# Performance work log

Measured on AMD Instinct MI355X. Metric: run time of the kernel, lower is better.

The kernel has to match this reference:

```python
import jax, jax.numpy as jnp
import numpy as np
import math

E = 1024   # embed_dim
H = 16     # num_heads
LAT = 1024 # latent_dim
P = LAT // 16  # projectionMatrice output dim (per-head width)
B = 2
S = 2048


def setup_inputs() -> dict:
    key = jax.random.key(0)
    ks = jax.random.split(key, 11)
    sc = 0.02  # small init scale so exp(dot(q_vec, k_vec)) stays finite
    return {
        "x": jax.random.normal(ks[0], (B, S, E), jnp.float32),
        "WQ": jax.random.normal(ks[1], (E, E), jnp.float32) * sc,
        "WK": jax.random.normal(ks[2], (E, E), jnp.float32) * sc,
        "WV": jax.random.normal(ks[3], (E, E), jnp.float32) * sc,
        "result_weight": jax.random.normal(ks[4], (E, E), jnp.float32) * sc,
        "proj_w": jax.random.normal(ks[5], (E, P), jnp.float32) * sc,
        "proj_b": jax.random.normal(ks[6], (P,), jnp.float32) * sc,
        "q1_vector": jax.random.normal(ks[7], (E,), jnp.float32) * sc,
        "k1_vector": jax.random.normal(ks[8], (E,), jnp.float32) * sc,
        "q2_vector": jax.random.normal(ks[9], (E,), jnp.float32) * sc,
        "k2_vector": jax.random.normal(ks[10], (E,), jnp.float32) * sc,
        "lambda_init": jnp.zeros((1,), jnp.float32),
    }


def reference(x, WQ, WK, WV, result_weight, proj_w, proj_b,
              q1_vector, k1_vector, q2_vector, k2_vector, lambda_init):
    head_dim = E // H
    scale = 1.0 / math.sqrt(head_dim)
    # projectionMatrice(x @ W): torch Linear -> x @ proj_w + proj_b with proj_w [E, P]
    q = (x @ WQ) @ proj_w + proj_b   # [B, S, P]
    k = (x @ WK) @ proj_w + proj_b   # [B, S, P]
    v = (x @ WV) @ proj_w + proj_b   # [B, S, P]
    q1, q2 = jnp.split(q, 2, axis=-1)  # [B, S, P/2] each
    k1, k2 = jnp.split(k, 2, axis=-1)
    lam = (jnp.exp(jnp.dot(q1_vector, k1_vector))
           - jnp.exp(jnp.dot(q2_vector, k2_vector)) + lambda_init[0])
    attn1 = jnp.einsum('bsp,btp->bst', q1, k1) * scale  # [B, S, S]
    attn2 = jnp.einsum('bsp,btp->bst', q2, k2) * scale
    base = jnp.einsum('bst,btp->bsp', attn1 - lam * attn2, v)  # [B, S, P]
    # Stateful KV-cache grows by one identical (key, value) copy per head call;
    # head i's tiled-cache output equals (i+1) * base (exact reassociation).
    mult = jnp.arange(1, H + 1, dtype=x.dtype)  # [H]
    heads = (base[:, :, None, :] * mult[None, None, :, None]).reshape(B, S, H * P)  # [B, S, E]
    return heads @ result_weight
```

## Files before the change

### kernel.cpp

```cpp
#include <hip/hip_runtime.h>
#include <hip/hip_bf16.h>


typedef __attribute__((ext_vector_type(8))) short short8;
typedef __attribute__((ext_vector_type(4))) float f32x4;
typedef unsigned short ushort_t;
typedef unsigned int uint_t;

__device__ inline ushort_t f2bf(float v) {
    uint_t u = __float_as_uint(v);
    return (ushort_t)((u + 0x7FFF + ((u >> 16) & 1)) >> 16);
}
__device__ inline float bf2f(ushort_t h) { return __uint_as_float(((uint_t)h) << 16); }
__device__ inline void split2(float v, ushort_t& hi, ushort_t& lo) {
    hi = f2bf(v);
    lo = f2bf(v - bf2f(hi));
}
__device__ inline int swzA(int row, int k) { return (row * 64 + k) ^ ((row & 7) << 3); }

__global__ __launch_bounds__(256) void prep_sk(
    const float* __restrict__ WQ, const float* __restrict__ WK, const float* __restrict__ WV,
    const float* __restrict__ proj_w, float* __restrict__ wppartT)
{
    __shared__ __align__(16) ushort_t Ah[4096], Al[4096], Bh[4096], Bl[4096];
    int bid = blockIdx.x;
    int slice = bid / 48, t = bid % 48, z = t / 16, rowblk = t % 16;
    const float* A = ((z == 0) ? WQ : (z == 1) ? WK : WV) + (long long)rowblk * 64 * 1024;

    int tid = threadIdx.x;
    int wave = tid >> 6, lane = tid & 63;
    int rl = lane & 15, kg = lane >> 4;
    f32x4 acc[4] = {};

    int k0 = slice * 128;
    for (int ch = 0; ch < 2; ++ch, k0 += 64) {
        #pragma unroll
        for (int i = 0; i < 4; ++i) {
            int pos = tid + 256 * i;
            int r = pos >> 4, k4 = (pos & 15) * 4;
            float4 v = *(const float4*)&A[(long long)r * 1024 + k0 + k4];
            ushort4 h, l;
            split2(v.x, h.x, l.x); split2(v.y, h.y, l.y);
            split2(v.z, h.z, l.z); split2(v.w, h.w, l.w);
            int idx = swzA(r, k4);
            *(ushort4*)&Ah[idx] = h;
            *(ushort4*)&Al[idx] = l;
        }
        #pragma unroll
        for (int i = 0; i < 4; ++i) {
            int pos = tid + 256 * i;
            int kk = pos >> 4, n4 = (pos & 15) * 4;
            float4 v = *(const float4*)&proj_w[(long long)(k0 + kk) * 64 + n4];
            float vv[4] = {v.x, v.y, v.z, v.w};
            #pragma unroll
            for (int j = 0; j < 4; ++j) {
                ushort_t h, l; split2(vv[j], h, l);
                int idx = swzA(n4 + j, kk);
                Bh[idx] = h; Bl[idx] = l;
            }
        }
        __syncthreads();
        int ar = wave * 16 + rl;
        #pragma unroll
        for (int ks = 0; ks < 2; ++ks) {
            int kb = ks * 32 + kg * 8;
            short8 ah = *(const short8*)&Ah[swzA(ar, kb)];
            short8 al = *(const short8*)&Al[swzA(ar, kb)];
            #pragma unroll
            for (int n = 0; n < 4; ++n) {
                int bi = swzA(n * 16 + rl, kb);
                short8 bh = *(const short8*)&Bh[bi];
                short8 bl = *(const short8*)&Bl[bi];
                acc[n] = __builtin_amdgcn_mfma_f32_16x16x32_bf16(ah, bh, acc[n], 0, 0, 0);
                acc[n] = __builtin_amdgcn_mfma_f32_16x16x32_bf16(ah, bl, acc[n], 0, 0, 0);
                acc[n] = __builtin_amdgcn_mfma_f32_16x16x32_bf16(al, bh, acc[n], 0, 0, 0);
            }
        }
        __syncthreads();
    }
    #pragma unroll
    for (int n = 0; n < 4; ++n) {
        int col = n * 16 + rl;
        float4 o = {acc[n][0], acc[n][1], acc[n][2], acc[n][3]};
        long long idx = (long long)slice * 196608 + (long long)(z * 64 + col) * 1024
                      + rowblk * 64 + wave * 16 + kg * 4;
        *(float4*)&wppartT[idx] = o;
    }
}

__global__ __launch_bounds__(256) void wpfix2(
    const float* __restrict__ wppartT,
    ushort_t* __restrict__ WpThi, ushort_t* __restrict__ WpTlo)
{
    int idx = blockIdx.x * 256 + threadIdx.x;
    long long off = (long long)idx * 4;
    float4 s = {0.f, 0.f, 0.f, 0.f};
    #pragma unroll
    for (int sl = 0; sl < 8; ++sl) {
        float4 m = *(const float4*)&wppartT[(long long)sl * 196608 + off];
        s.x += m.x; s.y += m.y; s.z += m.z; s.w += m.w;
    }
    ushort4 h, l;
    split2(s.x, h.x, l.x); split2(s.y, h.y, l.y);
    split2(s.z, h.z, l.z); split2(s.w, h.w, l.w);
    *(ushort4*)&WpThi[off] = h;
    *(ushort4*)&WpTlo[off] = l;
}

__global__ __launch_bounds__(256) void qkv2(
    const float* __restrict__ x,
    const ushort_t* __restrict__ WpThi, const ushort_t* __restrict__ WpTlo,
    const float* __restrict__ proj_b,
    ushort_t* __restrict__ Qhi, ushort_t* __restrict__ Qlo,
    float* __restrict__ kbuf, float* __restrict__ vbuf)
{
    __shared__ __align__(16) ushort_t Ah[4096], Al[4096], Bh[4096], Bl[4096];
    int bid = blockIdx.x, tid = threadIdx.x;
    int z = bid >> 6, rowblk = bid & 63;
    long long row0 = (long long)rowblk * 64;
    int wave = tid >> 6, lane = tid & 63, rl = lane & 15, kg = lane >> 4;
    f32x4 acc[4] = {};
    float4 av[4];
    short8 pbh[2], pbl[2];
    #pragma unroll
    for (int i = 0; i < 4; ++i) {
        int pos = tid + 256 * i;
        int r = pos >> 4, c4 = (pos & 15) * 4;
        av[i] = *(const float4*)&x[(row0 + r) * 1024 + c4];
    }
    #pragma unroll
    for (int i = 0; i < 2; ++i) {
        int pos = tid + 256 * i;
        int n = pos >> 3, k8 = (pos & 7) * 8;
        long long src = (long long)(z * 64 + n) * 1024 + k8;
        pbh[i] = *(const short8*)&WpThi[src];
        pbl[i] = *(const short8*)&WpTlo[src];
    }
    for (int ch = 0; ch < 16; ++ch) {
        #pragma unroll
        for (int i = 0; i < 4; ++i) {
            int pos = tid + 256 * i;
            int r = pos >> 4, c4 = (pos & 15) * 4;
            ushort4 h, l;
            split2(av[i].x, h.x, l.x); split2(av[i].y, h.y, l.y);
            split2(av[i].z, h.z, l.z); split2(av[i].w, h.w, l.w);
            int idx = swzA(r, c4);
            *(ushort4*)&Ah[idx] = h;
            *(ushort4*)&Al[idx] = l;
        }
        #pragma unroll
        for (int i = 0; i < 2; ++i) {
            int pos = tid + 256 * i;
            int n = pos >> 3, k8 = (pos & 7) * 8;
            int idx = swzA(n, k8);
            *(short8*)&Bh[idx] = pbh[i];
            *(short8*)&Bl[idx] = pbl[i];
        }
        __syncthreads();
        if (ch < 15) {
            int k0 = (ch + 1) * 64;
            #pragma unroll
            for (int i = 0; i < 4; ++i) {
                int pos = tid + 256 * i;
                int r = pos >> 4, c4 = (pos & 15) * 4;
                av[i] = *(const float4*)&x[(row0 + r) * 1024 + k0 + c4];
            }
            #pragma unroll
            for (int i = 0; i < 2; ++i) {
                int pos = tid + 256 * i;
                int n = pos >> 3, k8 = (pos & 7) * 8;
                long long src = (long long)(z * 64 + n) * 1024 + k0 + k8;
                pbh[i] = *(const short8*)&WpThi[src];
                pbl[i] = *(const short8*)&WpTlo[src];
            }
        }
        int ar = wave * 16 + rl;
        #pragma unroll
        for (int ks = 0; ks < 2; ++ks) {
            int kb = ks * 32 + kg * 8;
            short8 ah = *(const short8*)&Ah[swzA(ar, kb)];
            short8 al = *(const short8*)&Al[swzA(ar, kb)];
            #pragma unroll
            for (int n = 0; n < 4; ++n) {
                int bi = swzA(n * 16 + rl, kb);
                short8 bh = *(const short8*)&Bh[bi];
                short8 bl = *(const short8*)&Bl[bi];
                acc[n] = __builtin_amdgcn_mfma_f32_16x16x32_bf16(ah, bh, acc[n], 0, 0, 0);
                acc[n] = __builtin_amdgcn_mfma_f32_16x16x32_bf16(ah, bl, acc[n], 0, 0, 0);
                acc[n] = __builtin_amdgcn_mfma_f32_16x16x32_bf16(al, bh, acc[n], 0, 0, 0);
            }
        }
        __builtin_amdgcn_s_barrier();
    }
    #pragma unroll
    for (int n = 0; n < 4; ++n) {
        int col = n * 16 + rl;
        float bb = proj_b[col];
        #pragma unroll
        for (int j = 0; j < 4; ++j) {
            long long row = row0 + wave * 16 + kg * 4 + j;
            float val = acc[n][j] + bb;
            if (z == 0) {
                ushort_t h, l; split2(val, h, l);
                Qhi[row * 64 + col] = h;
                Qlo[row * 64 + col] = l;
            } else if (z == 1) {
                kbuf[row * 64 + col] = val;
            } else {
                vbuf[row * 64 + col] = val;
            }
        }
    }
}

__global__ __launch_bounds__(256) void mpart2(
    const float* __restrict__ kbuf, const float* __restrict__ vbuf,
    float* __restrict__ Mpart)
{
    int bid = blockIdx.x;
    int sc = bid & 63, b = bid >> 6;
    __shared__ float ksh[32][68], vsh[32][68];
    int tid = threadIdx.x;
    long long row0 = (long long)b * 2048 + sc * 32;
    #pragma unroll
    for (int i = 0; i < 4; ++i) {
        int pos = tid + 256 * i;
        int arr = pos >> 9, rem = pos & 511;
        int r = rem >> 4, c4 = (rem & 15) * 4;
        const float* src = (arr ? vbuf : kbuf) + (row0 + r) * 64 + c4;
        float4 v = *(const float4*)src;
        if (arr == 0) *(float4*)&ksh[r][c4] = v;
        else          *(float4*)&vsh[r][c4] = v;
    }
    __syncthreads();
    int p = tid & 63, cg = tid >> 6;
    float acc[16] = {};
    for (int s = 0; s < 32; ++s) {
        float vv = vsh[s][p];
        float4 k0 = *(const float4*)&ksh[s][cg * 16];
        float4 k1 = *(const float4*)&ksh[s][cg * 16 + 4];
        float4 k2 = *(const float4*)&ksh[s][cg * 16 + 8];
        float4 k3 = *(const float4*)&ksh[s][cg * 16 + 12];
        acc[0] += k0.x * vv;  acc[1] += k0.y * vv;  acc[2] += k0.z * vv;  acc[3] += k0.w * vv;
        acc[4] += k1.x * vv;  acc[5] += k1.y * vv;  acc[6] += k1.z * vv;  acc[7] += k1.w * vv;
        acc[8] += k2.x * vv;  acc[9] += k2.y * vv;  acc[10] += k2.z * vv; acc[11] += k2.w * vv;
        acc[12] += k3.x * vv; acc[13] += k3.y * vv; acc[14] += k3.z * vv; acc[15] += k3.w * vv;
    }
    float* o = Mpart + ((long long)b * 64 + sc) * 4096;
    #pragma unroll
    for (int ci = 0; ci < 16; ++ci)
        o[(cg * 16 + ci) * 64 + p] = acc[ci];
}

__global__ __launch_bounds__(256) void gkern3(
    const float* __restrict__ Mpart, const float* __restrict__ RW,
    const float* __restrict__ q1v, const float* __restrict__ k1v,
    const float* __restrict__ q2v, const float* __restrict__ k2v,
    const float* __restrict__ lam0,
    ushort_t* __restrict__ GThi, ushort_t* __restrict__ GTlo)
{
    int colblk = blockIdx.x & 15, b = blockIdx.x >> 4;
    __shared__ float As[64][68], Bs[64][68];
    __shared__ float red[2][4];
    int tid = threadIdx.x;

    float d1 = 0.f, d2 = 0.f;
    for (int i = tid; i < 1024; i += 256) {
        d1 += q1v[i] * k1v[i];
        d2 += q2v[i] * k2v[i];
    }
    #pragma unroll
    for (int off = 32; off > 0; off >>= 1) {
        d1 += __shfl_down(d1, off);
        d2 += __shfl_down(d2, off);
    }
    if ((tid & 63) == 0) { red[0][tid >> 6] = d1; red[1][tid >> 6] = d2; }
    __syncthreads();
    float s1 = red[0][0] + red[0][1] + red[0][2] + red[0][3];
    float s2 = red[1][0] + red[1][1] + red[1][2] + red[1][3];
    float lam = expf(s1) - expf(s2) + lam0[0];

    #pragma unroll
    for (int i = 0; i < 4; ++i) {
        int pos = tid + 256 * i;
        int c = pos >> 4, p4 = (pos & 15) * 4;
        float4 s = {0.f, 0.f, 0.f, 0.f};
        #pragma unroll 8
        for (int sc = 0; sc < 64; ++sc) {
            float4 m = *(const float4*)&Mpart[((long long)b * 64 + sc) * 4096 + c * 64 + p4];
            s.x += m.x; s.y += m.y; s.z += m.z; s.w += m.w;
        }
        float coef = 0.125f * (c < 32 ? 1.0f : -lam);
        s.x *= coef; s.y *= coef; s.z *= coef; s.w *= coef;
        *(float4*)&As[c][p4] = s;
    }
    #pragma unroll
    for (int i = 0; i < 4; ++i) {
        int pos = tid + 256 * i;
        int p = pos >> 4, e4 = (pos & 15) * 4;
        float4 s = {0.f, 0.f, 0.f, 0.f};
        #pragma unroll
        for (int h = 0; h < 16; ++h) {
            float4 r = *(const float4*)&RW[(long long)(h * 64 + p) * 1024 + colblk * 64 + e4];
            float m = (float)(h + 1);
            s.x += m * r.x; s.y += m * r.y; s.z += m * r.z; s.w += m * r.w;
        }
        *(float4*)&Bs[p][e4] = s;
    }
    __syncthreads();

    int tx = tid & 15, ty = tid >> 4;
    float acc[4][4] = {};
    #pragma unroll 4
    for (int kk4 = 0; kk4 < 64; kk4 += 4) {
        float4 a4[4], b4[4];
        #pragma unroll
        for (int i = 0; i < 4; ++i) a4[i] = *(const float4*)&As[ty * 4 + i][kk4];
        #pragma unroll
        for (int r = 0; r < 4; ++r) b4[r] = *(const float4*)&Bs[kk4 + r][tx * 4];
        #pragma unroll
        for (int i = 0; i < 4; ++i) {
            acc[i][0] += a4[i].x * b4[0].x + a4[i].y * b4[1].x + a4[i].z * b4[2].x + a4[i].w * b4[3].x;
            acc[i][1] += a4[i].x * b4[0].y + a4[i].y * b4[1].y + a4[i].z * b4[2].y + a4[i].w * b4[3].y;
            acc[i][2] += a4[i].x * b4[0].z + a4[i].y * b4[1].z + a4[i].z * b4[2].z + a4[i].w * b4[3].z;
            acc[i][3] += a4[i].x * b4[0].w + a4[i].y * b4[1].w + a4[i].z * b4[2].w + a4[i].w * b4[3].w;
        }
    }
    #pragma unroll
    for (int i = 0; i < 4; ++i)
        #pragma unroll
        for (int j = 0; j < 4; ++j) {
            ushort_t h, l; split2(acc[i][j], h, l);
            long long idx = (long long)b * 65536 + (long long)(colblk * 64 + tx * 4 + j) * 64 + ty * 4 + i;
            GThi[idx] = h; GTlo[idx] = l;
        }
}

__global__ __launch_bounds__(256) void outk(
    const ushort_t* __restrict__ Qhi, const ushort_t* __restrict__ Qlo,
    const ushort_t* __restrict__ GThi, const ushort_t* __restrict__ GTlo,
    float* __restrict__ out)
{
    __shared__ __align__(16) ushort_t Ah[4096], Al[4096], Bh[4096], Bl[4096];
    int bid = blockIdx.x;
    int rowblk = bid & 31, colblk = (bid >> 5) & 15, b = bid >> 9;
    int tid = threadIdx.x;
    long long row0 = (long long)b * 2048 + rowblk * 64;

    #pragma unroll
    for (int i = 0; i < 2; ++i) {
        int pos = tid + 256 * i;
        int n = pos >> 3, k8 = (pos & 7) * 8;
        int idx = swzA(n, k8);
        long long qsrc = (row0 + n) * 64 + k8;
        long long gsrc = (long long)b * 65536 + (long long)(colblk * 64 + n) * 64 + k8;
        *(short8*)&Ah[idx] = *(const short8*)&Qhi[qsrc];
        *(short8*)&Al[idx] = *(const short8*)&Qlo[qsrc];
        *(short8*)&Bh[idx] = *(const short8*)&GThi[gsrc];
        *(short8*)&Bl[idx] = *(const short8*)&GTlo[gsrc];
    }
    __syncthreads();

    int wave = tid >> 6, lane = tid & 63;
    int rl = lane & 15, kg = lane >> 4;
    f32x4 acc[4] = {};
    int ar = wave * 16 + rl;
    #pragma unroll
    for (int ks = 0; ks < 2; ++ks) {
        int kb = ks * 32 + kg * 8;
        short8 ah = *(const short8*)&Ah[swzA(ar, kb)];
        short8 al = *(const short8*)&Al[swzA(ar, kb)];
        #pragma unroll
        for (int n = 0; n < 4; ++n) {
            int bi = swzA(n * 16 + rl, kb);
            short8 bh = *(const short8*)&Bh[bi];
            short8 bl = *(const short8*)&Bl[bi];
            acc[n] = __builtin_amdgcn_mfma_f32_16x16x32_bf16(ah, bh, acc[n], 0, 0, 0);
            acc[n] = __builtin_amdgcn_mfma_f32_16x16x32_bf16(ah, bl, acc[n], 0, 0, 0);
            acc[n] = __builtin_amdgcn_mfma_f32_16x16x32_bf16(al, bh, acc[n], 0, 0, 0);
        }
    }
    #pragma unroll
    for (int n = 0; n < 4; ++n) {
        int col = colblk * 64 + n * 16 + rl;
        #pragma unroll
        for (int j = 0; j < 4; ++j) {
            int row = rowblk * 64 + wave * 16 + kg * 4 + j;
            out[(long long)b * 2097152 + (long long)row * 1024 + col] = acc[n][j];
        }
    }
}

extern "C" void kernel_launch(void* const* d_in, const int* in_sizes, int n_in,
                              void* d_out, int out_size, void* d_ws, size_t ws_size,
                              hipStream_t stream)
{
    const float* x      = (const float*)d_in[0];
    const float* WQ     = (const float*)d_in[1];
    const float* WK     = (const float*)d_in[2];
    const float* WV     = (const float*)d_in[3];
    const float* RW     = (const float*)d_in[4];
    const float* proj_w = (const float*)d_in[5];
    const float* proj_b = (const float*)d_in[6];
    const float* q1v    = (const float*)d_in[7];
    const float* k1v    = (const float*)d_in[8];
    const float* q2v    = (const float*)d_in[9];
    const float* k2v    = (const float*)d_in[10];
    const float* lam0   = (const float*)d_in[11];
    float* out = (float*)d_out;

    float* ws       = (float*)d_ws;
    float* wppartT  = ws;
    float* kbuf     = ws + 1572864;
    float* vbuf     = ws + 1835008;
    float* Mpart    = ws + 2097152;
    ushort_t* ub    = (ushort_t*)(ws + 2621440);
    ushort_t* WpThi = ub;
    ushort_t* WpTlo = ub + 196608;
    ushort_t* Qhi   = ub + 393216;
    ushort_t* Qlo   = ub + 655360;
    ushort_t* GThi  = ub + 917504;
    ushort_t* GTlo  = ub + 1048576;

    dim3 blk(256);
    prep_sk<<<dim3(384), blk, 0, stream>>>(WQ, WK, WV, proj_w, wppartT);
    wpfix2<<<dim3(192), blk, 0, stream>>>(wppartT, WpThi, WpTlo);
    qkv2<<<dim3(192), blk, 0, stream>>>(x, WpThi, WpTlo, proj_b, Qhi, Qlo, kbuf, vbuf);
    mpart2<<<dim3(128), blk, 0, stream>>>(kbuf, vbuf, Mpart);
    gkern3<<<dim3(32), blk, 0, stream>>>(Mpart, RW, q1v, k1v, q2v, k2v, lam0, GThi, GTlo);
    outk<<<dim3(1024), blk, 0, stream>>>(Qhi, Qlo, GThi, GTlo, out);
}
```

Baseline: 70.34 us.

## Move RW head-sum and lambda computation off the critical gkern into earlier kernel

The reduction of result_weight over heads with multipliers (h+1) and the lambda scalar were computed inside the 32-block gkern3, where each block redundantly re-read 16 rows of RW. They now run as extra blocks of the Wp fix-up kernel, writing Weff and lambda to the workspace, so the small 32-block kernel only loads the precomputed Weff tile. This spreads the RW read across 64 blocks in a wider kernel and shortens the serial low-occupancy stage, at the cost of an extra Weff round-trip through memory. Workspace pointers are now derived in-kernel via a macro.

Measured after the change: 73.65 us. 4.7% more time.

```diff
diff --git a/kernel.cpp b/kernel.cpp
--- a/kernel.cpp
+++ b/kernel.cpp
@@ -18,11 +18,29 @@
 }
 __device__ inline int swzA(int row, int k) { return (row * 64 + k) ^ ((row & 7) << 3); }
 
+#define WS_PTRS(ws) \
+    float* wppartT = (ws); \
+    float* kbuf    = (ws) + 1572864; \
+    float* vbuf    = (ws) + 1835008; \
+    float* Mpart   = (ws) + 2097152; \
+    float* Weff    = (ws) + 2621440; \
+    float* lamp    = (ws) + 2686976; \
+    ushort_t* ub   = (ushort_t*)((ws) + 2686992); \
+    ushort_t* WpThi = ub; \
+    ushort_t* WpTlo = ub + 196608; \
+    ushort_t* Qhi   = ub + 393216; \
+    ushort_t* Qlo   = ub + 655360; \
+    ushort_t* GThi  = ub + 917504; \
+    ushort_t* GTlo  = ub + 1048576;
+
 __global__ __launch_bounds__(256) void prep_sk(
     const float* __restrict__ WQ, const float* __restrict__ WK, const float* __restrict__ WV,
-    const float* __restrict__ proj_w, float* __restrict__ wppartT)
+    const float* __restrict__ proj_w, float* __restrict__ ws)
 {
     __shared__ __align__(16) ushort_t Ah[4096], Al[4096], Bh[4096], Bl[4096];
+    WS_PTRS(ws)
+    (void)kbuf; (void)vbuf; (void)Mpart; (void)Weff; (void)lamp;
+    (void)WpThi; (void)WpTlo; (void)Qhi; (void)Qlo; (void)GThi; (void)GTlo;
     int bid = blockIdx.x;
     int slice = bid / 48, t = bid % 48, z = t / 16, rowblk = t % 16;
     const float* A = ((z == 0) ? WQ : (z == 1) ? WK : WV) + (long long)rowblk * 64 * 1024;
@@ -88,33 +106,69 @@
     }
 }
 
-__global__ __launch_bounds__(256) void wpfix2(
-    const float* __restrict__ wppartT,
-    ushort_t* __restrict__ WpThi, ushort_t* __restrict__ WpTlo)
-{
-    int idx = blockIdx.x * 256 + threadIdx.x;
-    long long off = (long long)idx * 4;
-    float4 s = {0.f, 0.f, 0.f, 0.f};
-    #pragma unroll
-    for (int sl = 0; sl < 8; ++sl) {
-        float4 m = *(const float4*)&wppartT[(long long)sl * 196608 + off];
-        s.x += m.x; s.y += m.y; s.z += m.z; s.w += m.w;
-    }
-    ushort4 h, l;
-    split2(s.x, h.x, l.x); split2(s.y, h.y, l.y);
-    split2(s.z, h.z, l.z); split2(s.w, h.w, l.w);
-    *(ushort4*)&WpThi[off] = h;
-    *(ushort4*)&WpTlo[off] = l;
+__global__ __launch_bounds__(256) void wpfix2x(
+    const float* __restrict__ RW,
+    const float* __restrict__ q1v, const float* __restrict__ k1v,
+    const float* __restrict__ q2v, const float* __restrict__ k2v,
+    const float* __restrict__ lam0, float* __restrict__ ws)
+{
+    __shared__ float red[2][4];
+    WS_PTRS(ws)
+    (void)kbuf; (void)vbuf; (void)Mpart; (void)Qhi; (void)Qlo; (void)GThi; (void)GTlo;
+    int t = blockIdx.x, tid = threadIdx.x;
+    if (t < 192) {
+        int idx = t * 256 + tid;
+        long long off = (long long)idx * 4;
+        float4 s = {0.f, 0.f, 0.f, 0.f};
+        #pragma unroll
+        for (int sl = 0; sl < 8; ++sl) {
+            float4 m = *(const float4*)&wppartT[(long long)sl * 196608 + off];
+            s.x += m.x; s.y += m.y; s.z += m.z; s.w += m.w;
+        }
+        ushort4 h, l;
+        split2(s.x, h.x, l.x); split2(s.y, h.y, l.y);
+        split2(s.z, h.z, l.z); split2(s.w, h.w, l.w);
+        *(ushort4*)&WpThi[off] = h;
+        *(ushort4*)&WpTlo[off] = l;
+    } else if (t < 256) {
+        int f4i = (t - 192) * 256 + tid;
+        int p = f4i >> 8, e4 = (f4i & 255) * 4;
+        float4 s = {0.f, 0.f, 0.f, 0.f};
+        #pragma unroll
+        for (int h = 0; h < 16; ++h) {
+            float4 r = *(const float4*)&RW[(long long)(h * 64 + p) * 1024 + e4];
+            float m = (float)(h + 1);
+            s.x += m * r.x; s.y += m * r.y; s.z += m * r.z; s.w += m * r.w;
+        }
+        *(float4*)&Weff[(long long)p * 1024 + e4] = s;
+    } else {
+        float d1 = 0.f, d2 = 0.f;
+        for (int i = tid; i < 1024; i += 256) {
+            d1 += q1v[i] * k1v[i];
+            d2 += q2v[i] * k2v[i];
+        }
+        #pragma unroll
+        for (int off = 32; off > 0; off >>= 1) {
+            d1 += __shfl_down(d1, off);
+            d2 += __shfl_down(d2, off);
+        }
+        if ((tid & 63) == 0) { red[0][tid >> 6] = d1; red[1][tid >> 6] = d2; }
+        __syncthreads();
+        if (tid == 0) {
+            float s1 = red[0][0] + red[0][1] + red[0][2] + red[0][3];
+            float s2 = red[1][0] + red[1][1] + red[1][2] + red[1][3];
+            lamp[0] = expf(s1) - expf(s2) + lam0[0];
+        }
+    }
 }
 
 __global__ __launch_bounds__(256) void qkv2(
-    const float* __restrict__ x,
-    const ushort_t* __restrict__ WpThi, const ushort_t* __restrict__ WpTlo,
-    const float* __restrict__ proj_b,
-    ushort_t* __restrict__ Qhi, ushort_t* __restrict__ Qlo,
-    float* __restrict__ kbuf, float* __restrict__ vbuf)
+    const float* __restrict__ x, const float* __restrict__ proj_b,
+    float* __restrict__ ws)
 {
     __shared__ __align__(16) ushort_t Ah[4096], Al[4096], Bh[4096], Bl[4096];
+    WS_PTRS(ws)
+    (void)wppartT; (void)Mpart; (void)Weff; (void)lamp; (void)GThi; (void)GTlo;
     int bid = blockIdx.x, tid = threadIdx.x;
     int z = bid >> 6, rowblk = bid & 63;
     long long row0 = (long long)rowblk * 64;
@@ -213,13 +267,14 @@
     }
 }
 
-__global__ __launch_bounds__(256) void mpart2(
-    const float* __restrict__ kbuf, const float* __restrict__ vbuf,
-    float* __restrict__ Mpart)
-{
+__global__ __launch_bounds__(256) void mpart2(float* __restrict__ ws)
+{
+    __shared__ float ksh[32][68], vsh[32][68];
+    WS_PTRS(ws)
+    (void)wppartT; (void)Weff; (void)lamp; (void)WpThi; (void)WpTlo;
+    (void)Qhi; (void)Qlo; (void)GThi; (void)GTlo;
     int bid = blockIdx.x;
     int sc = bid & 63, b = bid >> 6;
-    __shared__ float ksh[32][68], vsh[32][68];
     int tid = threadIdx.x;
     long long row0 = (long long)b * 2048 + sc * 32;
     #pragma unroll
@@ -252,34 +307,14 @@
         o[(cg * 16 + ci) * 64 + p] = acc[ci];
 }
 
-__global__ __launch_bounds__(256) void gkern3(
-    const float* __restrict__ Mpart, const float* __restrict__ RW,
-    const float* __restrict__ q1v, const float* __restrict__ k1v,
-    const float* __restrict__ q2v, const float* __restrict__ k2v,
-    const float* __restrict__ lam0,
-    ushort_t* __restrict__ GThi, ushort_t* __restrict__ GTlo)
-{
-    int colblk = blockIdx.x & 15, b = blockIdx.x >> 4;
+__global__ __launch_bounds__(256) void meffgk(float* __restrict__ ws)
+{
     __shared__ float As[64][68], Bs[64][68];
-    __shared__ float red[2][4];
-    int tid = threadIdx.x;
-
-    float d1 = 0.f, d2 = 0.f;
-    for (int i = tid; i < 1024; i += 256) {
-        d1 += q1v[i] * k1v[i];
-        d2 += q2v[i] * k2v[i];
-    }
-    #pragma unroll
-    for (int off = 32; off > 0; off >>= 1) {
-        d1 += __shfl_down(d1, off);
-        d2 += __shfl_down(d2, off);
-    }
-    if ((tid & 63) == 0) { red[0][tid >> 6] = d1; red[1][tid >> 6] = d2; }
-    __syncthreads();
-    float s1 = red[0][0] + red[0][1] + red[0][2] + red[0][3];
-    float s2 = red[1][0] + red[1][1] + red[1][2] + red[1][3];
-    float lam = expf(s1) - expf(s2) + lam0[0];
-
+    WS_PTRS(ws)
+    (void)wppartT; (void)kbuf; (void)vbuf; (void)WpThi; (void)WpTlo; (void)Qhi; (void)Qlo;
+    int t = blockIdx.x, tid = threadIdx.x;
+    int colblk = t & 15, b = t >> 4;
+    float lam = lamp[0];
     #pragma unroll
     for (int i = 0; i < 4; ++i) {
         int pos = tid + 256 * i;
@@ -298,17 +333,9 @@
     for (int i = 0; i < 4; ++i) {
         int pos = tid + 256 * i;
         int p = pos >> 4, e4 = (pos & 15) * 4;
-        float4 s = {0.f, 0.f, 0.f, 0.f};
-        #pragma unroll
-        for (int h = 0; h < 16; ++h) {
-            float4 r = *(const float4*)&RW[(long long)(h * 64 + p) * 1024 + colblk * 64 + e4];
-            float m = (float)(h + 1);
-            s.x += m * r.x; s.y += m * r.y; s.z += m * r.z; s.w += m * r.w;
-        }
-        *(float4*)&Bs[p][e4] = s;
+        *(float4*)&Bs[p][e4] = *(const float4*)&Weff[(long long)p * 1024 + colblk * 64 + e4];
     }
     __syncthreads();
-
     int tx = tid & 15, ty = tid >> 4;
     float acc[4][4] = {};
     #pragma unroll 4
@@ -336,12 +363,12 @@
         }
 }
 
-__global__ __launch_bounds__(256) void outk(
-    const ushort_t* __restrict__ Qhi, const ushort_t* __restrict__ Qlo,
-    const ushort_t* __restrict__ GThi, const ushort_t* __restrict__ GTlo,
-    float* __restrict__ out)
+__global__ __launch_bounds__(256) void outk(float* __restrict__ ws, float* __restrict__ out)
 {
     __shared__ __align__(16) ushort_t Ah[4096], Al[4096], Bh[4096], Bl[4096];
+    WS_PTRS(ws)
+    (void)wppartT; (void)kbuf; (void)vbuf; (void)Mpart; (void)Weff; (void)lamp;
+    (void)WpThi; (void)WpTlo;
     int bid = blockIdx.x;
     int rowblk = bid & 31, colblk = (bid >> 5) & 15, b = bid >> 9;
     int tid = threadIdx.x;
@@ -407,26 +434,14 @@
     const float* q2v    = (const float*)d_in[9];
     const float* k2v    = (const float*)d_in[10];
     const float* lam0   = (const float*)d_in[11];
+    float* ws  = (float*)d_ws;
     float* out = (float*)d_out;
 
-    float* ws       = (float*)d_ws;
-    float* wppartT  = ws;
-    float* kbuf     = ws + 1572864;
-    float* vbuf     = ws + 1835008;
-    float* Mpart    = ws + 2097152;
-    ushort_t* ub    = (ushort_t*)(ws + 2621440);
-    ushort_t* WpThi = ub;
-    ushort_t* WpTlo = ub + 196608;
-    ushort_t* Qhi   = ub + 393216;
-    ushort_t* Qlo   = ub + 655360;
-    ushort_t* GThi  = ub + 917504;
-    ushort_t* GTlo  = ub + 1048576;
-
     dim3 blk(256);
-    prep_sk<<<dim3(384), blk, 0, stream>>>(WQ, WK, WV, proj_w, wppartT);
-    wpfix2<<<dim3(192), blk, 0, stream>>>(wppartT, WpThi, WpTlo);
-    qkv2<<<dim3(192), blk, 0, stream>>>(x, WpThi, WpTlo, proj_b, Qhi, Qlo, kbuf, vbuf);
-    mpart2<<<dim3(128), blk, 0, stream>>>(kbuf, vbuf, Mpart);
-    gkern3<<<dim3(32), blk, 0, stream>>>(Mpart, RW, q1v, k1v, q2v, k2v, lam0, GThi, GTlo);
-    outk<<<dim3(1024), blk, 0, stream>>>(Qhi, Qlo, GThi, GTlo, out);
-}
+    prep_sk<<<dim3(384), blk, 0, stream>>>(WQ, WK, WV, proj_w, ws);
+    wpfix2x<<<dim3(257), blk, 0, stream>>>(RW, q1v, k1v, q2v, k2v, lam0, ws);
+    qkv2<<<dim3(192), blk, 0, stream>>>(x, proj_b, ws);
+    mpart2<<<dim3(128), blk, 0, stream>>>(ws);
+    meffgk<<<dim3(32), blk, 0, stream>>>(ws);
+    outk<<<dim3(1024), blk, 0, stream>>>(ws, out);
+}
```
